# Kernel optimization log

Measured on AMD Instinct MI355X. Metric: run time of the kernel, lower is better.

Reference implementation:

```python
import jax, jax.numpy as jnp
import numpy as np

D = 1024   # embed_dim
H = 16     # n_heads
DH = D // H
B, N = 4, 1024


def setup_inputs() -> dict:
    key = jax.random.key(0)
    k0, k1, k2 = jax.random.split(key, 3)
    x = jax.random.normal(k0, (B, N, D), jnp.float32)
    # Per-head kqv Linear weights batched: each head maps D -> 2*D + D//H
    Wkqv = jax.random.normal(k1, (H, D, 2 * D + DH), jnp.float32) * 0.02
    bkqv = jnp.zeros((H, 2 * D + DH), jnp.float32)
    Wp = jax.random.normal(k2, (D, D), jnp.float32) * 0.02
    bp = jnp.zeros((D,), jnp.float32)
    return {"x": x, "Wkqv": Wkqv, "bkqv": bkqv, "Wp": Wp, "bp": bp}


def reference(x, Wkqv, bkqv, Wp, bp):
    Bm, Nm, Dm = x.shape
    # batched per-head projections: y[b,h,n,:] = x[b,n,:] @ Wkqv[h] + bkqv[h]
    y = jnp.einsum('bnd,hde->bhne', x, Wkqv) + bkqv[None, :, None, :]
    k = y[..., :Dm]          # [B,H,N,D]  (full embed_dim per head, as in source)
    q = y[..., Dm:2 * Dm]    # [B,H,N,D]
    v = y[..., 2 * Dm:]      # [B,H,N,DH]
    # attention_scores: q @ k^T / sqrt(D) -- scale uses FULL embed_dim (faithful)
    A = jnp.einsum('bhnd,bhmd->bhnm', q, k) / jnp.sqrt(jnp.float32(Dm))
    mask = jnp.tril(jnp.ones((Nm, Nm), dtype=bool))
    A = jnp.where(mask[None, None], A, -jnp.inf)
    A = jax.nn.softmax(A, axis=-1)
    sa = jnp.einsum('bhnm,bhmd->bnhd', A, v).reshape(Bm, Nm, Dm)
    return sa @ Wp + bp
```

## Files before the change

### kernel.cpp

```cpp
#include <hip/hip_runtime.h>
#include <hip/hip_bf16.h>

#define B_ 4
#define N_ 1024
#define D_ 1024
#define H_ 16
#define DH_ 64
#define E_ 2112
#define ROWS_ 4096

typedef __bf16 bf16_t;
typedef bf16_t bf16x4 __attribute__((ext_vector_type(4)));
typedef bf16_t bf16x8 __attribute__((ext_vector_type(8)));
typedef float f32x4 __attribute__((ext_vector_type(4)));

__device__ __forceinline__ void gload_lds16(const void* g, void* l) {
  __builtin_amdgcn_global_load_lds(
      (const __attribute__((address_space(1))) void*)g,
      (__attribute__((address_space(3))) void*)l, 16, 0, 0);
}

__global__ __launch_bounds__(256)
void conv_x(const float* __restrict__ x, bf16_t* __restrict__ xb) {
  const int n4 = ROWS_ * D_ / 4;
  for (int i = blockIdx.x * 256 + threadIdx.x; i < n4; i += gridDim.x * 256) {
    float4 v = ((const float4*)x)[i];
    bf16x4 o = {(bf16_t)v.x, (bf16_t)v.y, (bf16_t)v.z, (bf16_t)v.w};
    ((bf16x4*)xb)[i] = o;
  }
}

__global__ __launch_bounds__(256)
void conv_wqk(const float* __restrict__ W, const float* __restrict__ bkqv,
              bf16_t* __restrict__ Wqb, bf16_t* __restrict__ Wkb,
              float* __restrict__ wqbk, float* __restrict__ wkbq) {
  const int db = blockIdx.x;
  const int h = blockIdx.y;
  const float* Wh = W + (size_t)h * D_ * E_;
  __shared__ float bq[1024], bk[1024];
  __shared__ float red[2][16][17];
  const int t = threadIdx.x;
  for (int i = t; i < 1024; i += 256) {
    bk[i] = bkqv[h * E_ + i];
    bq[i] = bkqv[h * E_ + 1024 + i];
  }
  __syncthreads();
  const int rt = t >> 4, ct = t & 15;
  const int d = db * 16 + rt;
  const float* rowp = Wh + (size_t)d * E_;
  float pk = 0.f, pq = 0.f;
  #pragma unroll
  for (int j = 0; j < 16; ++j) {
    int e4 = (ct + j * 16) * 4;
    float4 vk = *(const float4*)(rowp + e4);
    float4 vq = *(const float4*)(rowp + 1024 + e4);
    bf16x4 ok = {(bf16_t)vk.x, (bf16_t)vk.y, (bf16_t)vk.z, (bf16_t)vk.w};
    bf16x4 oq = {(bf16_t)vq.x, (bf16_t)vq.y, (bf16_t)vq.z, (bf16_t)vq.w};
    *(bf16x4*)(Wkb + ((size_t)h * 1024 + d) * 1024 + e4) = ok;
    *(bf16x4*)(Wqb + ((size_t)h * 1024 + d) * 1024 + e4) = oq;
    pk += vk.x * bq[e4] + vk.y * bq[e4 + 1] + vk.z * bq[e4 + 2] + vk.w * bq[e4 + 3];
    pq += vq.x * bk[e4] + vq.y * bk[e4 + 1] + vq.z * bk[e4 + 2] + vq.w * bk[e4 + 3];
  }
  red[0][rt][ct] = pk;
  red[1][rt][ct] = pq;
  __syncthreads();
  if (t < 32) {
    int which = t >> 4, r = t & 15;
    float s = 0.f;
    #pragma unroll
    for (int c2 = 0; c2 < 16; ++c2) s += red[which][r][c2];
    if (which == 0) wkbq[h * 1024 + db * 16 + r] = s;
    else            wqbk[h * 1024 + db * 16 + r] = s;
  }
}

__global__ __launch_bounds__(256)
void bqk_kernel(const float* __restrict__ bkqv, float* __restrict__ bqk) {
  const int h = blockIdx.x;
  const int t = threadIdx.x;
  __shared__ float red[256];
  const float* bk = bkqv + h * E_;
  const float* bq = bk + 1024;
  float4 a = *(const float4*)(bk + t * 4);
  float4 b = *(const float4*)(bq + t * 4);
  red[t] = a.x * b.x + a.y * b.y + a.z * b.z + a.w * b.w;
  __syncthreads();
  for (int st = 128; st > 0; st >>= 1) {
    if (t < st) red[t] += red[t + st];
    __syncthreads();
  }
  if (t == 0) bqk[h] = red[0];
}

__global__ __launch_bounds__(256)
void uv_kernel(const float* __restrict__ x, const float* __restrict__ bqk,
               const float* __restrict__ wqbk, const float* __restrict__ wkbq,
               float* __restrict__ u, float* __restrict__ v) {
  const int t = threadIdx.x;
  const int w = t >> 6, l = t & 63;
  const int rg = blockIdx.x * 4 + w;
  const int b = rg >> 10, n = rg & 1023;
  const float* xr = x + (size_t)rg * 1024 + l * 16;
  float4 xv0 = *(const float4*)(xr);
  float4 xv1 = *(const float4*)(xr + 4);
  float4 xv2 = *(const float4*)(xr + 8);
  float4 xv3 = *(const float4*)(xr + 12);
  #pragma unroll
  for (int h = 0; h < 16; ++h) {
    const float* wq = wqbk + h * 1024 + l * 16;
    const float* wk = wkbq + h * 1024 + l * 16;
    float4 q0 = *(const float4*)(wq);
    float4 q1 = *(const float4*)(wq + 4);
    float4 q2 = *(const float4*)(wq + 8);
    float4 q3 = *(const float4*)(wq + 12);
    float4 k0 = *(const float4*)(wk);
    float4 k1 = *(const float4*)(wk + 4);
    float4 k2 = *(const float4*)(wk + 8);
    float4 k3 = *(const float4*)(wk + 12);
    float au = xv0.x * q0.x + xv0.y * q0.y + xv0.z * q0.z + xv0.w * q0.w
             + xv1.x * q1.x + xv1.y * q1.y + xv1.z * q1.z + xv1.w * q1.w
             + xv2.x * q2.x + xv2.y * q2.y + xv2.z * q2.z + xv2.w * q2.w
             + xv3.x * q3.x + xv3.y * q3.y + xv3.z * q3.z + xv3.w * q3.w;
    float av = xv0.x * k0.x + xv0.y * k0.y + xv0.z * k0.z + xv0.w * k0.w
             + xv1.x * k1.x + xv1.y * k1.y + xv1.z * k1.z + xv1.w * k1.w
             + xv2.x * k2.x + xv2.y * k2.y + xv2.z * k2.z + xv2.w * k2.w
             + xv3.x * k3.x + xv3.y * k3.y + xv3.z * k3.z + xv3.w * k3.w;
    #pragma unroll
    for (int s = 1; s < 64; s <<= 1) {
      au += __shfl_xor(au, s);
      av += __shfl_xor(av, s);
    }
    if (l == 0) {
      int bh = b * 16 + h;
      u[(size_t)bh * 1024 + n] = au + bqk[h];
      v[(size_t)bh * 1024 + n] = av;
    }
  }
}

__global__ __launch_bounds__(256)
void conv_wv(const float* __restrict__ W, bf16_t* __restrict__ Wvt) {
  const int et = blockIdx.x, dt = blockIdx.y, h = blockIdx.z;
  const int tx = threadIdx.x & 31, ty = threadIdx.x >> 5;
  __shared__ float tile[32][33];
  const float* Wh = W + (size_t)h * D_ * E_;
  #pragma unroll
  for (int rr = 0; rr < 4; ++rr) {
    int d = dt * 32 + rr * 8 + ty;
    int dh = et * 32 + tx;
    tile[rr * 8 + ty][tx] = Wh[(size_t)d * E_ + 2048 + dh];
  }
  __syncthreads();
  bf16_t* Wvo = Wvt + (size_t)h * DH_ * D_;
  #pragma unroll
  for (int rr = 0; rr < 4; ++rr) {
    int dh = et * 32 + rr * 8 + ty;
    int d = dt * 32 + tx;
    Wvo[(size_t)dh * D_ + d] = (bf16_t)tile[tx][rr * 8 + ty];
  }
}

__global__ __launch_bounds__(256)
void conv_wp(const float* __restrict__ Wp, bf16_t* __restrict__ Wpt) {
  const int nt = blockIdx.x, kt = blockIdx.y;
  const int tx = threadIdx.x & 31, ty = threadIdx.x >> 5;
  __shared__ float tile[32][33];
  #pragma unroll
  for (int rr = 0; rr < 4; ++rr)
    tile[rr * 8 + ty][tx] = Wp[(size_t)(kt * 32 + rr * 8 + ty) * D_ + nt * 32 + tx];
  __syncthreads();
  #pragma unroll
  for (int rr = 0; rr < 4; ++rr)
    Wpt[(size_t)(nt * 32 + rr * 8 + ty) * D_ + kt * 32 + tx] = (bf16_t)tile[tx][rr * 8 + ty];
}

__global__ __launch_bounds__(256)
void v_gemm(const bf16_t* __restrict__ xb, const bf16_t* __restrict__ Wvt,
            const float* __restrict__ bkqv, bf16_t* __restrict__ Vt) {
  const int nt = blockIdx.x;
  const int h = blockIdx.y;
  const int t = threadIdx.x;
  const int w = t >> 6, l = t & 63, l15 = l & 15, lg = l >> 4;

  __shared__ bf16_t As2[64 * 64];
  __shared__ bf16_t Bs2[128 * 64];
  const bf16_t* Wvh = Wvt + (size_t)h * DH_ * D_;
  const bf16_t* Bn = xb + (size_t)nt * 128 * D_;

  f32x4 acc[4][2] = {};
  const int rswz = (l15 & 7) << 4;

  for (int kb = 0; kb < 16; ++kb) {
    __syncthreads();
    #pragma unroll
    for (int i = 0; i < 2; ++i) {
      int idx = t + i * 256;
      int row = idx >> 3, c = idx & 7;
      gload_lds16(Wvh + (size_t)row * D_ + kb * 64 + ((c ^ (row & 7)) << 3),
                  (char*)As2 + idx * 16);
    }
    #pragma unroll
    for (int i = 0; i < 4; ++i) {
      int idx = t + i * 256;
      int row = idx >> 3, c = idx & 7;
      gload_lds16(Bn + (size_t)row * D_ + kb * 64 + ((c ^ (row & 7)) << 3),
                  (char*)Bs2 + idx * 16);
    }
    __syncthreads();
    #pragma unroll
    for (int ks = 0; ks < 2; ++ks) {
      const int cswz = (ks * 64 + lg * 16) ^ rswz;
      bf16x8 a[4], b[2];
      #pragma unroll
      for (int mi = 0; mi < 4; ++mi)
        a[mi] = *(const bf16x8*)((const char*)As2 + (mi * 16 + l15) * 128 + cswz);
      #pragma unroll
      for (int ni = 0; ni < 2; ++ni)
        b[ni] = *(const bf16x8*)((const char*)Bs2 + (w * 32 + ni * 16 + l15) * 128 + cswz);
      #pragma unroll
      for (int mi = 0; mi < 4; ++mi)
        #pragma unroll
        for (int ni = 0; ni < 2; ++ni)
          acc[mi][ni] = __builtin_amdgcn_mfma_f32_16x16x32_bf16(a[mi], b[ni], acc[mi][ni], 0, 0, 0);
    }
  }

  #pragma unroll
  for (int mi = 0; mi < 4; ++mi)
    #pragma unroll
    for (int r = 0; r < 4; ++r) {
      int dh = mi * 16 + lg * 4 + r;
      float bias = bkqv[h * E_ + 2048 + dh];
      #pragma unroll
      for (int ni = 0; ni < 2; ++ni) {
        int nn = nt * 128 + w * 32 + ni * 16 + l15;
        int b = nn >> 10, n = nn & (N_ - 1);
        int bh = b * H_ + h;
        Vt[((size_t)bh * DH_ + dh) * N_ + n] = (bf16_t)(acc[mi][ni][r] + bias);
      }
    }
}

#define WV8 asm volatile("s_waitcnt vmcnt(8)" ::: "memory")
#define WV2 asm volatile("s_waitcnt vmcnt(2)" ::: "memory")
#define WV0 asm volatile("s_waitcnt vmcnt(0)" ::: "memory")
#define WNONE

__device__ __forceinline__ void mm256_core(const bf16_t* __restrict__ Ag,
                                           const bf16_t* __restrict__ Bg,
                                           bf16_t* lds, f32x4 (&acc)[8][4]) {
  char* Asp = (char*)lds;
  char* Bsp = (char*)lds + 65536;
  const int t = threadIdx.x;
  const int w = t >> 6, l = t & 63, l15 = l & 15, lg = l >> 4;
  const int wm = w >> 2, wn = w & 3;

  const int lr = l >> 3;
  const int scol = ((l & 7) ^ lr) << 3;
  const bf16_t* bS = Bg + (size_t)(w * 8 + lr) * 1024 + scol;
  const int idxA = w * 8 + lr;
  const bf16_t* aS0 = Ag + (size_t)((idxA >> 4) * 32 + (idxA & 15)) * 1024 + scol;
  const bf16_t* aS1 = aS0 + (size_t)128 * 1024;

#define STG_B(bufi, hh, ktv)                                                   \
  do {                                                                         \
    gload_lds16(bS + (size_t)((hh) * 128) * 1024 + (ktv) * 64,                 \
                Bsp + (bufi) * 32768 + (hh) * 16384 + w * 1024);               \
    gload_lds16(bS + (size_t)((hh) * 128 + 64) * 1024 + (ktv) * 64,            \
                Bsp + (bufi) * 32768 + (hh) * 16384 + 8192 + w * 1024);        \
  } while (0)
#define STG_A(bufi, hh, ktv)                                                   \
  do {                                                                         \
    gload_lds16(aS0 + (size_t)((hh) * 16) * 1024 + (ktv) * 64,                 \
                Asp + (bufi) * 32768 + (hh) * 16384 + w * 1024);               \
    gload_lds16(aS1 + (size_t)((hh) * 16) * 1024 + (ktv) * 64,                 \
                Asp + (bufi) * 32768 + (hh) * 16384 + 8192 + w * 1024);        \
  } while (0)

  STG_B(0, 0, 0); STG_B(0, 1, 0);
  STG_A(0, 0, 0); STG_A(0, 1, 0);
  STG_B(1, 0, 1); STG_B(1, 1, 1);
  STG_A(1, 0, 1);
  WV8;
  __builtin_amdgcn_s_barrier();

  const int rswz = (l15 & 7) << 4;
  const int bro = ((wn & 1) * 64 + l15) * 128;

#define TILE_STEP(KT, SA1, SB, SA0, W1, W3)                                    \
  {                                                                            \
    const int kb_ = (KT) & 1;                                                  \
    const char* Ab = Asp + kb_ * 32768;                                        \
    const char* Bb = Bsp + kb_ * 32768 + (wn >> 1) * 16384;                    \
    bf16x8 b0[4], b1[4];                                                       \
    {                                                                          \
      const int cs = (lg * 16) ^ rswz;                                         \
      bf16x8 a[4];                                                             \
      _Pragma("unroll") for (int ni = 0; ni < 4; ++ni)                         \
        b0[ni] = *(const bf16x8*)(Bb + bro + ni * 2048 + cs);                  \
      _Pragma("unroll") for (int q = 0; q < 4; ++q)                            \
        a[q] = *(const bf16x8*)(Ab + ((wm * 4 + q) * 16 + l15) * 128 + cs);    \
      if (SA1) STG_A(((KT) + 1) & 1, 1, (KT) + 1);                             \
      asm volatile("s_waitcnt lgkmcnt(0)" ::: "memory");                       \
      __builtin_amdgcn_s_setprio(1);                                           \
      _Pragma("unroll") for (int q = 0; q < 4; ++q)                            \
        _Pragma("unroll") for (int ni = 0; ni < 4; ++ni)                       \
          acc[2 * q][ni] = __builtin_amdgcn_mfma_f32_16x16x32_bf16(            \
              a[q], b0[ni], acc[2 * q][ni], 0, 0, 0);                          \
      __builtin_amdgcn_s_setprio(0);                                           \
      __builtin_amdgcn_s_barrier();                                            \
    }                                                                          \
    {                                                                          \
      const int cs = (64 + lg * 16) ^ rswz;                                    \
      bf16x8 a[4];                                                             \
      _Pragma("unroll") for (int ni = 0; ni < 4; ++ni)                         \
        b1[ni] = *(const bf16x8*)(Bb + bro + ni * 2048 + cs);                  \
      _Pragma("unroll") for (int q = 0; q < 4; ++q)                            \
        a[q] = *(const bf16x8*)(Ab + ((wm * 4 + q) * 16 + l15) * 128 + cs);    \
      asm volatile("s_waitcnt lgkmcnt(0)" ::: "memory");                       \
      __builtin_amdgcn_s_setprio(1);                                           \
      _Pragma("unroll") for (int q = 0; q < 4; ++q)                            \
        _Pragma("unroll") for (int ni = 0; ni < 4; ++ni)                       \
          acc[2 * q][ni] = __builtin_amdgcn_mfma_f32_16x16x32_bf16(            \
              a[q], b1[ni], acc[2 * q][ni], 0, 0, 0);                          \
      __builtin_amdgcn_s_setprio(0);                                           \
      W1;                                                                      \
      __builtin_amdgcn_s_barrier();                                            \
    }                                                                          \
    {                                                                          \
      const int cs = (lg * 16) ^ rswz;                                         \
      bf16x8 a[4];                                                             \
      _Pragma("unroll") for (int q = 0; q < 4; ++q)                            \
        a[q] = *(const bf16x8*)(Ab + 16384 + ((wm * 4 + q) * 16 + l15) * 128 + cs); \
      if (SB) { STG_B((KT) & 1, 0, (KT) + 2); STG_B((KT) & 1, 1, (KT) + 2); }  \
      asm volatile("s_waitcnt lgkmcnt(0)" ::: "memory");                       \
      __builtin_amdgcn_s_setprio(1);                                           \
      _Pragma("unroll") for (int q = 0; q < 4; ++q)                            \
        _Pragma("unroll") for (int ni = 0; ni < 4; ++ni)                       \
          acc[2 * q + 1][ni] = __builtin_amdgcn_mfma_f32_16x16x32_bf16(        \
              a[q], b0[ni], acc[2 * q + 1][ni], 0, 0, 0);                      \
      __builtin_amdgcn_s_setprio(0);                                           \
      __builtin_amdgcn_s_barrier();                                            \
    }                                                                          \
    {                                                                          \
      const int cs = (64 + lg * 16) ^ rswz;                                    \
      bf16x8 a[4];                                                             \
      _Pragma("unroll") for (int q = 0; q < 4; ++q)                            \
        a[q] = *(const bf16x8*)(Ab + 16384 + ((wm * 4 + q) * 16 + l15) * 128 + cs); \
      if (SA0) STG_A((KT) & 1, 0, (KT) + 2);                                   \
      asm volatile("s_waitcnt lgkmcnt(0)" ::: "memory");                       \
      __builtin_amdgcn_s_setprio(1);                                           \
      _Pragma("unroll") for (int q = 0; q < 4; ++q)                            \
        _Pragma("unroll") for (int ni = 0; ni < 4; ++ni)                       \
          acc[2 * q + 1][ni] = __builtin_amdgcn_mfma_f32_16x16x32_bf16(        \
              a[q], b1[ni], acc[2 * q + 1][ni], 0, 0, 0);                      \
      __builtin_amdgcn_s_setprio(0);                                           \
      W3;                                                                      \
      __builtin_amdgcn_s_barrier();                                            \
    }                                                                          \
  }

  for (int kt = 0; kt < 14; ++kt) TILE_STEP(kt, 1, 1, 1, WV8, WV8);
  TILE_STEP(14, 1, 0, 0, WV8, WV2);
  TILE_STEP(15, 0, 0, 0, WV0, WNONE);

#undef TILE_STEP
#undef STG_A
#undef STG_B
}

__device__ __forceinline__ int xchunk4(int colf) {
  int c = colf >> 2;
  return ((c ^ (c >> 3)) << 2) | (colf & 3);
}

__device__ __forceinline__ void epi256_bf16(f32x4 (&acc)[8][4], bf16_t* lds,
                                            bf16_t* dst) {
  const int t = threadIdx.x;
  const int l = t & 63, l15 = l & 15, lg = l >> 4;
  const int w = t >> 6;
  const int wm = w >> 2, wn = w & 3;
  float* Ct = (float*)lds;
  const int cpair = t & 31;
  const int p0 = xchunk4(cpair * 8);
  const int p1 = xchunk4(cpair * 8 + 4);
  #pragma unroll
  for (int s = 0; s < 4; ++s) {
    __syncthreads();
    #pragma unroll
    for (int m2 = 0; m2 < 2; ++m2)
      #pragma unroll
      for (int ni = 0; ni < 4; ++ni)
        #pragma unroll
        for (int r = 0; r < 4; ++r)
          Ct[(wm * 32 + m2 * 16 + lg * 4 + r) * 258 +
             xchunk4(wn * 64 + ni * 16 + l15)] = acc[2 * s + m2][ni][r];
    __syncthreads();
    #pragma unroll
    for (int it = 0; it < 4; ++it) {
      int row64 = (t >> 5) + it * 16;
      int wmq = row64 >> 5, m2q = (row64 >> 4) & 1, r16 = row64 & 15;
      int c8 = cpair * 8;
      const float* r0 = &Ct[row64 * 258 + p0];
      const float* r1 = &Ct[row64 * 258 + p1];
      bf16x8 o = {(bf16_t)r0[0], (bf16_t)r0[1], (bf16_t)r0[2], (bf16_t)r0[3],
                  (bf16_t)r1[0], (bf16_t)r1[1], (bf16_t)r1[2], (bf16_t)r1[3]};
      int lrow = wmq * 128 + (2 * s + m2q) * 16 + r16;
      *(bf16x8*)(dst + (size_t)lrow * 1024 + c8) = o;
    }
  }
}

__global__ __launch_bounds__(512)
void m_gemm(const bf16_t* __restrict__ Wkb, const bf16_t* __restrict__ Wqb,
            bf16_t* __restrict__ MT) {
  __shared__ bf16_t lds[65536];
  const int bid = blockIdx.x;
  const int mb = bid & 3, nb = (bid >> 2) & 3, h = bid >> 4;
  f32x4 acc[8][4] = {};
  mm256_core(Wkb + ((size_t)h * 1024 + mb * 256) * 1024,
             Wqb + ((size_t)h * 1024 + nb * 256) * 1024, lds, acc);
  epi256_bf16(acc, lds,
              MT + ((size_t)h * 1024 + mb * 256) * 1024 + nb * 256);
}

__global__ __launch_bounds__(512)
void t_gemm(const bf16_t* __restrict__ xb, const bf16_t* __restrict__ MT,
            bf16_t* __restrict__ T) {
  __shared__ bf16_t lds[65536];
  const int bid = blockIdx.x;
  const int lid = (bid & 7) * 128 + (bid >> 3);
  const int mb = lid & 15, nb = (lid >> 4) & 3, h = lid >> 6;
  f32x4 acc[8][4] = {};
  mm256_core(xb + (size_t)mb * 256 * 1024,
             MT + ((size_t)h * 1024 + nb * 256) * 1024, lds, acc);
  const int b = mb >> 2;
  const int bh = b * 16 + h;
  epi256_bf16(acc, lds,
              T + (size_t)bh * 1024 * 1024 + (size_t)((mb & 3) * 256) * 1024 +
                  nb * 256);
}

__global__ __launch_bounds__(512)
void s_gemm256(const bf16_t* __restrict__ T, const bf16_t* __restrict__ xb,
               const float* __restrict__ u, const float* __restrict__ v,
               float* __restrict__ SgC, int bh0) {
  __shared__ bf16_t lds[65536];
  const int bid = blockIdx.x;
  const int lid = (bid & 7) * 40 + (bid >> 3);
  const int idx = lid % 10;
  const int bhl = lid / 10;
  const int bh = bh0 + bhl;
  const int bb = bh >> 4;
  int qt = 0;
  while ((qt + 1) * (qt + 2) / 2 <= idx) ++qt;
  const int kt = idx - qt * (qt + 1) / 2;

  f32x4 acc[8][4] = {};
  mm256_core(T + (size_t)bh * 1024 * 1024 + (size_t)qt * 256 * 1024,
             xb + (size_t)bb * 1024 * 1024 + (size_t)kt * 256 * 1024, lds, acc);

  const int t = threadIdx.x;
  const int w = t >> 6, l = t & 63, l15 = l & 15, lg = l >> 4;
  const int wm = w >> 2, wn = w & 3;
  const float SCALE = 0.045084220027780106f;
  float* So = SgC + (((size_t)bhl * 10 + idx) << 16);

  const float* ubh = u + (size_t)bh * 1024 + qt * 256;
  const float* vbh = v + (size_t)bh * 1024 + kt * 256;
  float vv[4];
  #pragma unroll
  for (int ni = 0; ni < 4; ++ni) vv[ni] = vbh[wn * 64 + ni * 16 + l15];

  #pragma unroll
  for (int mi = 0; mi < 8; ++mi)
    #pragma unroll
    for (int r = 0; r < 4; ++r) {
      int rl = wm * 128 + mi * 16 + lg * 4 + r;
      float uu = ubh[rl];
      #pragma unroll
      for (int ni = 0; ni < 4; ++ni) {
        int cl = wn * 64 + ni * 16 + l15;
        float z = (acc[mi][ni][r] + uu + vv[ni]) * SCALE;
        if (kt * 256 + cl > qt * 256 + rl) z = -1e30f;
        acc[mi][ni][r] = z;
      }
    }

  float* Ct = (float*)lds;
  const int cpair = t & 31;
  const int p0 = xchunk4(cpair * 8);
  const int p1 = xchunk4(cpair * 8 + 4);
  #pragma unroll
  for (int s = 0; s < 4; ++s) {
    __syncthreads();
    #pragma unroll
    for (int m2 = 0; m2 < 2; ++m2)
      #pragma unroll
      for (int ni = 0; ni < 4; ++ni)
        #pragma unroll
        for (int r = 0; r < 4; ++r)
          Ct[(wm * 32 + m2 * 16 + lg * 4 + r) * 258 +
             xchunk4(wn * 64 + ni * 16 + l15)] = acc[2 * s + m2][ni][r];
    __syncthreads();
    #pragma unroll
    for (int it = 0; it < 4; ++it) {
      int row64 = (t >> 5) + it * 16;
      int wmq = row64 >> 5, m2q = (row64 >> 4) & 1, r16 = row64 & 15;
      int c8 = cpair * 8;
      const float* r0 = &Ct[row64 * 258 + p0];
      const float* r1 = &Ct[row64 * 258 + p1];
      float4 v0 = {r0[0], r0[1], r0[2], r0[3]};
      float4 v1 = {r1[0], r1[1], r1[2], r1[3]};
      int rl = wmq * 128 + (2 * s + m2q) * 16 + r16;
      *(float4*)(So + (size_t)rl * 256 + c8) = v0;
      *(float4*)(So + (size_t)rl * 256 + c8 + 4) = v1;
    }
  }
}

__global__ __launch_bounds__(256)
void softmax_pv(const float* __restrict__ SgC, const bf16_t* __restrict__ Vt,
                bf16_t* __restrict__ sa, int bh0) {
  const int qt = blockIdx.x;
  const int bhl = blockIdx.y;
  const int t = threadIdx.x;
  const int w = t >> 6, l = t & 63, l15 = l & 15, lg = l >> 4;
  const int bh = bh0 + bhl;
  const int b = bh >> 4, h = bh & 15;

  const int qrow = qt * 64 + w * 16 + l15;
  const int qt8 = qt >> 2;
  const float* Sbh = SgC + (((size_t)bhl * 10) << 16);
  const bf16_t* Vh = Vt + (size_t)bh * DH_ * N_;

  f32x4 accO[4] = {};
  float m = -1e30f, lsum = 0.f;

  for (int j = 0; j <= qt; ++j) {
    const int jb = j * 64;
    const int tid = qt8 * (qt8 + 1) / 2 + (j >> 2);
    const float* Srow = Sbh + ((size_t)tid << 16) + (size_t)(qrow & 255) * 256 + (jb & 255);

    float4 sA = *(const float4*)(Srow + lg * 8);
    float4 sB = *(const float4*)(Srow + lg * 8 + 4);
    float4 sC = *(const float4*)(Srow + 32 + lg * 8);
    float4 sD = *(const float4*)(Srow + 32 + lg * 8 + 4);

    float zm = fmaxf(fmaxf(fmaxf(sA.x, sA.y), fmaxf(sA.z, sA.w)),
                     fmaxf(fmaxf(sB.x, sB.y), fmaxf(sB.z, sB.w)));
    zm = fmaxf(zm, fmaxf(fmaxf(fmaxf(sC.x, sC.y), fmaxf(sC.z, sC.w)),
                         fmaxf(fmaxf(sD.x, sD.y), fmaxf(sD.z, sD.w))));
    zm = fmaxf(zm, __shfl_xor(zm, 16));
    zm = fmaxf(zm, __shfl_xor(zm, 32));

    float mnew = fmaxf(m, zm);
    float scl = exp2f(m - mnew);
    m = mnew;

    float p[16];
    p[0] = exp2f(sA.x - mnew); p[1] = exp2f(sA.y - mnew);
    p[2] = exp2f(sA.z - mnew); p[3] = exp2f(sA.w - mnew);
    p[4] = exp2f(sB.x - mnew); p[5] = exp2f(sB.y - mnew);
    p[6] = exp2f(sB.z - mnew); p[7] = exp2f(sB.w - mnew);
    p[8] = exp2f(sC.x - mnew); p[9] = exp2f(sC.y - mnew);
    p[10] = exp2f(sC.z - mnew); p[11] = exp2f(sC.w - mnew);
    p[12] = exp2f(sD.x - mnew); p[13] = exp2f(sD.y - mnew);
    p[14] = exp2f(sD.z - mnew); p[15] = exp2f(sD.w - mnew);

    float rs = 0.f;
    #pragma unroll
    for (int i = 0; i < 16; ++i) rs += p[i];
    rs += __shfl_xor(rs, 16);
    rs += __shfl_xor(rs, 32);
    lsum = lsum * scl + rs;

    float sclO[4];
    #pragma unroll
    for (int r = 0; r < 4; ++r) sclO[r] = __shfl(scl, lg * 4 + r);
    #pragma unroll
    for (int db = 0; db < 4; ++db)
      #pragma unroll
      for (int r = 0; r < 4; ++r) accO[db][r] *= sclO[r];

    bf16x8 pa0 = {(bf16_t)p[0], (bf16_t)p[1], (bf16_t)p[2], (bf16_t)p[3],
                  (bf16_t)p[4], (bf16_t)p[5], (bf16_t)p[6], (bf16_t)p[7]};
    bf16x8 pa1 = {(bf16_t)p[8], (bf16_t)p[9], (bf16_t)p[10], (bf16_t)p[11],
                  (bf16_t)p[12], (bf16_t)p[13], (bf16_t)p[14], (bf16_t)p[15]};

    #pragma unroll
    for (int db = 0; db < 4; ++db) {
      const bf16_t* vp = Vh + (size_t)(db * 16 + l15) * N_ + jb;
      bf16x8 vb0 = *(const bf16x8*)(vp + lg * 8);
      bf16x8 vb1 = *(const bf16x8*)(vp + 32 + lg * 8);
      accO[db] = __builtin_amdgcn_mfma_f32_16x16x32_bf16(pa0, vb0, accO[db], 0, 0, 0);
      accO[db] = __builtin_amdgcn_mfma_f32_16x16x32_bf16(pa1, vb1, accO[db], 0, 0, 0);
    }
  }

  float lO[4];
  #pragma unroll
  for (int r = 0; r < 4; ++r) lO[r] = __shfl(lsum, lg * 4 + r);

  #pragma unroll
  for (int db = 0; db < 4; ++db)
    #pragma unroll
    for (int r = 0; r < 4; ++r) {
      int row = qt * 64 + w * 16 + lg * 4 + r;
      int col = h * DH_ + db * 16 + l15;
      sa[((size_t)b * N_ + row) * D_ + col] = (bf16_t)(accO[db][r] / lO[r]);
    }
}

__global__ __launch_bounds__(256)
void out_gemm(const bf16_t* __restrict__ A, const bf16_t* __restrict__ Bt,
              const float* __restrict__ bp, float* __restrict__ out) {
  const int mb = blockIdx.x, nb = blockIdx.y;
  const int t = threadIdx.x;
  const int w = t >> 6, l = t & 63, l15 = l & 15, lg = l >> 4;
  const int wr = (w >> 1) * 64, wc = (w & 1) * 64;

  __shared__ bf16_t As[128 * 64];
  __shared__ bf16_t Bs[128 * 64];

  const int srow = w * 32 + (l >> 3);
  const int scol = (l & 7) * 8;
  const bf16_t* ag = A + (size_t)(mb * 128 + srow) * D_ + scol;
  const bf16_t* bg = Bt + (size_t)(nb * 128 + srow) * D_ + scol;
  char* asl = (char*)As + w * 4096;
  char* bsl = (char*)Bs + w * 4096;

  f32x4 acc[4][4] = {};

  for (int kb = 0; kb < 16; ++kb) {
    __syncthreads();
    #pragma unroll
    for (int i = 0; i < 4; ++i) {
      gload_lds16(ag + (size_t)i * 8 * D_ + kb * 64, asl + i * 1024);
      gload_lds16(bg + (size_t)i * 8 * D_ + kb * 64, bsl + i * 1024);
    }
    __syncthreads();
    #pragma unroll
    for (int ks = 0; ks < 2; ++ks) {
      bf16x8 a[4], b[4];
      #pragma unroll
      for (int mi = 0; mi < 4; ++mi)
        a[mi] = *(const bf16x8*)((const char*)As + (wr + mi * 16 + l15) * 128 + ks * 64 + lg * 16);
      #pragma unroll
      for (int ni = 0; ni < 4; ++ni)
        b[ni] = *(const bf16x8*)((const char*)Bs + (wc + ni * 16 + l15) * 128 + ks * 64 + lg * 16);
      #pragma unroll
      for (int mi = 0; mi < 4; ++mi)
        #pragma unroll
        for (int ni = 0; ni < 4; ++ni)
          acc[mi][ni] = __builtin_amdgcn_mfma_f32_16x16x32_bf16(a[mi], b[ni], acc[mi][ni], 0, 0, 0);
    }
  }

  #pragma unroll
  for (int ni = 0; ni < 4; ++ni) {
    int e = nb * 128 + wc + ni * 16 + l15;
    float bias = bp[e];
    #pragma unroll
    for (int mi = 0; mi < 4; ++mi)
      #pragma unroll
      for (int r = 0; r < 4; ++r) {
        int grow = mb * 128 + wr + mi * 16 + lg * 4 + r;
        out[(size_t)grow * D_ + e] = acc[mi][ni][r] + bias;
      }
  }
}

extern "C" void kernel_launch(void* const* d_in, const int* in_sizes, int n_in,
                              void* d_out, int out_size, void* d_ws, size_t ws_size,
                              hipStream_t stream) {
  const float* x    = (const float*)d_in[0];
  const float* Wkqv = (const float*)d_in[1];
  const float* bkqv = (const float*)d_in[2];
  const float* Wp   = (const float*)d_in[3];
  const float* bp   = (const float*)d_in[4];
  float* out = (float*)d_out;
  char* ws = (char*)d_ws;

  const size_t MB = 1 << 20;
  bf16_t* xb   = (bf16_t*)(ws);
  bf16_t* sa   = (bf16_t*)(ws + 8 * MB);
  bf16_t* Wpt  = (bf16_t*)(ws + 16 * MB);
  bf16_t* Vt   = (bf16_t*)(ws + 18 * MB);
  bf16_t* Wvt  = (bf16_t*)(ws + 26 * MB);
  bf16_t* MT   = (bf16_t*)(ws + 28 * MB);
  bf16_t* T    = (bf16_t*)(ws + 60 * MB);
  bf16_t* Wqb  = (bf16_t*)(ws + 188 * MB);
  bf16_t* Wkb  = (bf16_t*)(ws + 220 * MB);
  float*  SgC  = (float*) (ws + 188 * MB);
  float*  u    = (float*) (ws + 268 * MB);
  float*  v    = (float*) (ws + 268 * MB + 256 * 1024);
  float*  wqbk = (float*) (ws + 268 * MB + 512 * 1024);
  float*  wkbq = (float*) (ws + 268 * MB + 576 * 1024);
  float*  bqk  = (float*) (ws + 268 * MB + 640 * 1024);

  hipLaunchKernelGGL(conv_x, dim3(1024), dim3(256), 0, stream, x, xb);
  hipLaunchKernelGGL(conv_wp, dim3(32, 32), dim3(256), 0, stream, Wp, Wpt);
  hipLaunchKernelGGL(conv_wv, dim3(2, 32, 16), dim3(256), 0, stream, Wkqv, Wvt);
  hipLaunchKernelGGL(v_gemm, dim3(32, 16), dim3(256), 0, stream, xb, Wvt, bkqv, Vt);

  hipLaunchKernelGGL(conv_wqk, dim3(64, 16), dim3(256), 0, stream,
                     Wkqv, bkqv, Wqb, Wkb, wqbk, wkbq);
  hipLaunchKernelGGL(bqk_kernel, dim3(16), dim3(256), 0, stream, bkqv, bqk);
  hipLaunchKernelGGL(uv_kernel, dim3(1024), dim3(256), 0, stream,
                     x, bqk, wqbk, wkbq, u, v);
  hipLaunchKernelGGL(m_gemm, dim3(256), dim3(512), 0, stream, Wkb, Wqb, MT);
  hipLaunchKernelGGL(t_gemm, dim3(1024), dim3(512), 0, stream, xb, MT, T);

  for (int c = 0; c < 2; ++c) {
    hipLaunchKernelGGL(s_gemm256, dim3(320), dim3(512), 0, stream,
                       T, xb, u, v, SgC, c * 32);
    hipLaunchKernelGGL(softmax_pv, dim3(16, 32), dim3(256), 0, stream,
                       SgC, Vt, sa, c * 32);
  }

  hipLaunchKernelGGL(out_gemm, dim3(32, 8), dim3(256), 0, stream, sa, Wpt, bp, out);
}
```

Baseline: 516.8 us.

## Store attention scores in bf16, drop chunking, and merge prep kernels

```diff
diff --git a/kernel.cpp b/kernel.cpp
--- a/kernel.cpp
+++ b/kernel.cpp
@@ -21,12 +21,65 @@
 }
 
 __global__ __launch_bounds__(256)
-void conv_x(const float* __restrict__ x, bf16_t* __restrict__ xb) {
-  const int n4 = ROWS_ * D_ / 4;
-  for (int i = blockIdx.x * 256 + threadIdx.x; i < n4; i += gridDim.x * 256) {
-    float4 v = ((const float4*)x)[i];
-    bf16x4 o = {(bf16_t)v.x, (bf16_t)v.y, (bf16_t)v.z, (bf16_t)v.w};
-    ((bf16x4*)xb)[i] = o;
+void prep_all(const float* __restrict__ x, const float* __restrict__ Wp,
+              const float* __restrict__ W, const float* __restrict__ bkqv,
+              bf16_t* __restrict__ xb, bf16_t* __restrict__ Wpt,
+              bf16_t* __restrict__ Wvt, float* __restrict__ bqk) {
+  __shared__ float smem[1056];
+  const int bid = blockIdx.x;
+  const int t = threadIdx.x;
+  if (bid < 1024) {
+    const int n4 = ROWS_ * D_ / 4;
+    for (int i = bid * 256 + t; i < n4; i += 1024 * 256) {
+      float4 v = ((const float4*)x)[i];
+      bf16x4 o = {(bf16_t)v.x, (bf16_t)v.y, (bf16_t)v.z, (bf16_t)v.w};
+      ((bf16x4*)xb)[i] = o;
+    }
+  } else if (bid < 2048) {
+    const int id = bid - 1024;
+    const int nt = id & 31, kt = id >> 5;
+    const int tx = t & 31, ty = t >> 5;
+    #pragma unroll
+    for (int rr = 0; rr < 4; ++rr)
+      smem[(rr * 8 + ty) * 33 + tx] =
+          Wp[(size_t)(kt * 32 + rr * 8 + ty) * D_ + nt * 32 + tx];
+    __syncthreads();
+    #pragma unroll
+    for (int rr = 0; rr < 4; ++rr)
+      Wpt[(size_t)(nt * 32 + rr * 8 + ty) * D_ + kt * 32 + tx] =
+          (bf16_t)smem[tx * 33 + rr * 8 + ty];
+  } else if (bid < 3072) {
+    const int id = bid - 2048;
+    const int et = id & 1, dt = (id >> 1) & 31, h = id >> 6;
+    const int tx = t & 31, ty = t >> 5;
+    const float* Wh = W + (size_t)h * D_ * E_;
+    #pragma unroll
+    for (int rr = 0; rr < 4; ++rr) {
+      int d = dt * 32 + rr * 8 + ty;
+      int dh = et * 32 + tx;
+      smem[(rr * 8 + ty) * 33 + tx] = Wh[(size_t)d * E_ + 2048 + dh];
+    }
+    __syncthreads();
+    bf16_t* Wvo = Wvt + (size_t)h * DH_ * D_;
+    #pragma unroll
+    for (int rr = 0; rr < 4; ++rr) {
+      int dh = et * 32 + rr * 8 + ty;
+      int d = dt * 32 + tx;
+      Wvo[(size_t)dh * D_ + d] = (bf16_t)smem[tx * 33 + rr * 8 + ty];
+    }
+  } else {
+    const int h = bid - 3072;
+    const float* bk = bkqv + h * E_;
+    const float* bq = bk + 1024;
+    float4 a = *(const float4*)(bk + t * 4);
+    float4 b = *(const float4*)(bq + t * 4);
+    smem[t] = a.x * b.x + a.y * b.y + a.z * b.z + a.w * b.w;
+    __syncthreads();
+    for (int st = 128; st > 0; st >>= 1) {
+      if (t < st) smem[t] += smem[t + st];
+      __syncthreads();
+    }
+    if (t == 0) bqk[h] = smem[0];
   }
 }
 
@@ -72,24 +125,6 @@
     if (which == 0) wkbq[h * 1024 + db * 16 + r] = s;
     else            wqbk[h * 1024 + db * 16 + r] = s;
   }
-}
-
-__global__ __launch_bounds__(256)
-void bqk_kernel(const float* __restrict__ bkqv, float* __restrict__ bqk) {
-  const int h = blockIdx.x;
-  const int t = threadIdx.x;
-  __shared__ float red[256];
-  const float* bk = bkqv + h * E_;
-  const float* bq = bk + 1024;
-  float4 a = *(const float4*)(bk + t * 4);
-  float4 b = *(const float4*)(bq + t * 4);
-  red[t] = a.x * b.x + a.y * b.y + a.z * b.z + a.w * b.w;
-  __syncthreads();
-  for (int st = 128; st > 0; st >>= 1) {
-    if (t < st) red[t] += red[t + st];
-    __syncthreads();
-  }
-  if (t == 0) bqk[h] = red[0];
 }
 
 __global__ __launch_bounds__(256)
@@ -136,42 +171,6 @@
       v[(size_t)bh * 1024 + n] = av;
     }
   }
-}
-
-__global__ __launch_bounds__(256)
-void conv_wv(const float* __restrict__ W, bf16_t* __restrict__ Wvt) {
-  const int et = blockIdx.x, dt = blockIdx.y, h = blockIdx.z;
-  const int tx = threadIdx.x & 31, ty = threadIdx.x >> 5;
-  __shared__ float tile[32][33];
-  const float* Wh = W + (size_t)h * D_ * E_;
-  #pragma unroll
-  for (int rr = 0; rr < 4; ++rr) {
-    int d = dt * 32 + rr * 8 + ty;
-    int dh = et * 32 + tx;
-    tile[rr * 8 + ty][tx] = Wh[(size_t)d * E_ + 2048 + dh];
-  }
-  __syncthreads();
-  bf16_t* Wvo = Wvt + (size_t)h * DH_ * D_;
-  #pragma unroll
-  for (int rr = 0; rr < 4; ++rr) {
-    int dh = et * 32 + rr * 8 + ty;
-    int d = dt * 32 + tx;
-    Wvo[(size_t)dh * D_ + d] = (bf16_t)tile[tx][rr * 8 + ty];
-  }
-}
-
-__global__ __launch_bounds__(256)
-void conv_wp(const float* __restrict__ Wp, bf16_t* __restrict__ Wpt) {
-  const int nt = blockIdx.x, kt = blockIdx.y;
-  const int tx = threadIdx.x & 31, ty = threadIdx.x >> 5;
-  __shared__ float tile[32][33];
-  #pragma unroll
-  for (int rr = 0; rr < 4; ++rr)
-    tile[rr * 8 + ty][tx] = Wp[(size_t)(kt * 32 + rr * 8 + ty) * D_ + nt * 32 + tx];
-  __syncthreads();
-  #pragma unroll
-  for (int rr = 0; rr < 4; ++rr)
-    Wpt[(size_t)(nt * 32 + rr * 8 + ty) * D_ + kt * 32 + tx] = (bf16_t)tile[tx][rr * 8 + ty];
 }
 
 __global__ __launch_bounds__(256)
@@ -444,13 +443,12 @@
 __global__ __launch_bounds__(512)
 void s_gemm256(const bf16_t* __restrict__ T, const bf16_t* __restrict__ xb,
                const float* __restrict__ u, const float* __restrict__ v,
-               float* __restrict__ SgC, int bh0) {
+               bf16_t* __restrict__ Sg) {
   __shared__ bf16_t lds[65536];
   const int bid = blockIdx.x;
-  const int lid = (bid & 7) * 40 + (bid >> 3);
+  const int lid = (bid & 7) * 80 + (bid >> 3);
   const int idx = lid % 10;
-  const int bhl = lid / 10;
-  const int bh = bh0 + bhl;
+  const int bh = lid / 10;
   const int bb = bh >> 4;
   int qt = 0;
   while ((qt + 1) * (qt + 2) / 2 <= idx) ++qt;
@@ -464,7 +462,7 @@
   const int w = t >> 6, l = t & 63, l15 = l & 15, lg = l >> 4;
   const int wm = w >> 2, wn = w & 3;
   const float SCALE = 0.045084220027780106f;
-  float* So = SgC + (((size_t)bhl * 10 + idx) << 16);
+  bf16_t* So = Sg + (((size_t)bh * 10 + idx) << 16);
 
   const float* ubh = u + (size_t)bh * 1024 + qt * 256;
   const float* vbh = v + (size_t)bh * 1024 + kt * 256;
@@ -510,28 +508,26 @@
       int c8 = cpair * 8;
       const float* r0 = &Ct[row64 * 258 + p0];
       const float* r1 = &Ct[row64 * 258 + p1];
-      float4 v0 = {r0[0], r0[1], r0[2], r0[3]};
-      float4 v1 = {r1[0], r1[1], r1[2], r1[3]};
+      bf16x8 o = {(bf16_t)r0[0], (bf16_t)r0[1], (bf16_t)r0[2], (bf16_t)r0[3],
+                  (bf16_t)r1[0], (bf16_t)r1[1], (bf16_t)r1[2], (bf16_t)r1[3]};
       int rl = wmq * 128 + (2 * s + m2q) * 16 + r16;
-      *(float4*)(So + (size_t)rl * 256 + c8) = v0;
-      *(float4*)(So + (size_t)rl * 256 + c8 + 4) = v1;
+      *(bf16x8*)(So + (size_t)rl * 256 + c8) = o;
     }
   }
 }
 
 __global__ __launch_bounds__(256)
-void softmax_pv(const float* __restrict__ SgC, const bf16_t* __restrict__ Vt,
-                bf16_t* __restrict__ sa, int bh0) {
+void softmax_pv(const bf16_t* __restrict__ Sg, const bf16_t* __restrict__ Vt,
+                bf16_t* __restrict__ sa) {
   const int qt = blockIdx.x;
-  const int bhl = blockIdx.y;
+  const int bh = blockIdx.y;
   const int t = threadIdx.x;
   const int w = t >> 6, l = t & 63, l15 = l & 15, lg = l >> 4;
-  const int bh = bh0 + bhl;
   const int b = bh >> 4, h = bh & 15;
 
   const int qrow = qt * 64 + w * 16 + l15;
   const int qt8 = qt >> 2;
-  const float* Sbh = SgC + (((size_t)bhl * 10) << 16);
+  const bf16_t* Sbh = Sg + (((size_t)bh * 10) << 16);
   const bf16_t* Vh = Vt + (size_t)bh * DH_ * N_;
 
   f32x4 accO[4] = {};
@@ -540,17 +536,20 @@
   for (int j = 0; j <= qt; ++j) {
     const int jb = j * 64;
     const int tid = qt8 * (qt8 + 1) / 2 + (j >> 2);
-    const float* Srow = Sbh + ((size_t)tid << 16) + (size_t)(qrow & 255) * 256 + (jb & 255);
-
-    float4 sA = *(const float4*)(Srow + lg * 8);
-    float4 sB = *(const float4*)(Srow + lg * 8 + 4);
-    float4 sC = *(const float4*)(Srow + 32 + lg * 8);
-    float4 sD = *(const float4*)(Srow + 32 + lg * 8 + 4);
-
-    float zm = fmaxf(fmaxf(fmaxf(sA.x, sA.y), fmaxf(sA.z, sA.w)),
-                     fmaxf(fmaxf(sB.x, sB.y), fmaxf(sB.z, sB.w)));
-    zm = fmaxf(zm, fmaxf(fmaxf(fmaxf(sC.x, sC.y), fmaxf(sC.z, sC.w)),
-                         fmaxf(fmaxf(sD.x, sD.y), fmaxf(sD.z, sD.w))));
+    const bf16_t* Srow = Sbh + ((size_t)tid << 16) +
+                         (size_t)(qrow & 255) * 256 + (jb & 255);
+
+    bf16x8 h0 = *(const bf16x8*)(Srow + lg * 8);
+    bf16x8 h1 = *(const bf16x8*)(Srow + 32 + lg * 8);
+    float z[16];
+    #pragma unroll
+    for (int i = 0; i < 8; ++i) z[i] = (float)h0[i];
+    #pragma unroll
+    for (int i = 0; i < 8; ++i) z[8 + i] = (float)h1[i];
+
+    float zm = z[0];
+    #pragma unroll
+    for (int i = 1; i < 16; ++i) zm = fmaxf(zm, z[i]);
     zm = fmaxf(zm, __shfl_xor(zm, 16));
     zm = fmaxf(zm, __shfl_xor(zm, 32));
 
@@ -559,14 +558,8 @@
     m = mnew;
 
     float p[16];
-    p[0] = exp2f(sA.x - mnew); p[1] = exp2f(sA.y - mnew);
-    p[2] = exp2f(sA.z - mnew); p[3] = exp2f(sA.w - mnew);
-    p[4] = exp2f(sB.x - mnew); p[5] = exp2f(sB.y - mnew);
-    p[6] = exp2f(sB.z - mnew); p[7] = exp2f(sB.w - mnew);
-    p[8] = exp2f(sC.x - mnew); p[9] = exp2f(sC.y - mnew);
-    p[10] = exp2f(sC.z - mnew); p[11] = exp2f(sC.w - mnew);
-    p[12] = exp2f(sD.x - mnew); p[13] = exp2f(sD.y - mnew);
-    p[14] = exp2f(sD.z - mnew); p[15] = exp2f(sD.w - mnew);
+    #pragma unroll
+    for (int i = 0; i < 16; ++i) p[i] = exp2f(z[i] - mnew);
 
     float rs = 0.f;
     #pragma unroll
@@ -692,32 +685,27 @@
   bf16_t* T    = (bf16_t*)(ws + 60 * MB);
   bf16_t* Wqb  = (bf16_t*)(ws + 188 * MB);
   bf16_t* Wkb  = (bf16_t*)(ws + 220 * MB);
-  float*  SgC  = (float*) (ws + 188 * MB);
+  bf16_t* Sg   = (bf16_t*)(ws + 188 * MB);
   float*  u    = (float*) (ws + 268 * MB);
   float*  v    = (float*) (ws + 268 * MB + 256 * 1024);
   float*  wqbk = (float*) (ws + 268 * MB + 512 * 1024);
   float*  wkbq = (float*) (ws + 268 * MB + 576 * 1024);
   float*  bqk  = (float*) (ws + 268 * MB + 640 * 1024);
 
-  hipLaunchKernelGGL(conv_x, dim3(1024), dim3(256), 0, stream, x, xb);
-  hipLaunchKernelGGL(conv_wp, dim3(32, 32), dim3(256), 0, stream, Wp, Wpt);
-  hipLaunchKernelGGL(conv_wv, dim3(2, 32, 16), dim3(256), 0, stream, Wkqv, Wvt);
-  hipLaunchKernelGGL(v_gemm, dim3(32, 16), dim3(256), 0, stream, xb, Wvt, bkqv, Vt);
-
+  hipLaunchKernelGGL(prep_all, dim3(3088), dim3(256), 0, stream,
+                     x, Wp, Wkqv, bkqv, xb, Wpt, Wvt, bqk);
   hipLaunchKernelGGL(conv_wqk, dim3(64, 16), dim3(256), 0, stream,
                      Wkqv, bkqv, Wqb, Wkb, wqbk, wkbq);
-  hipLaunchKernelGGL(bqk_kernel, dim3(16), dim3(256), 0, stream, bkqv, bqk);
   hipLaunchKernelGGL(uv_kernel, dim3(1024), dim3(256), 0, stream,
                      x, bqk, wqbk, wkbq, u, v);
+  hipLaunchKernelGGL(v_gemm, dim3(32, 16), dim3(256), 0, stream,
+                     xb, Wvt, bkqv, Vt);
   hipLaunchKernelGGL(m_gemm, dim3(256), dim3(512), 0, stream, Wkb, Wqb, MT);
   hipLaunchKernelGGL(t_gemm, dim3(1024), dim3(512), 0, stream, xb, MT, T);
-
-  for (int c = 0; c < 2; ++c) {
-    hipLaunchKernelGGL(s_gemm256, dim3(320), dim3(512), 0, stream,
-                       T, xb, u, v, SgC, c * 32);
-    hipLaunchKernelGGL(softmax_pv, dim3(16, 32), dim3(256), 0, stream,
-                       SgC, Vt, sa, c * 32);
-  }
-
-  hipLaunchKernelGGL(out_gemm, dim3(32, 8), dim3(256), 0, stream, sa, Wpt, bp, out);
-}
+  hipLaunchKernelGGL(s_gemm256, dim3(640), dim3(512), 0, stream,
+                     T, xb, u, v, Sg);
+  hipLaunchKernelGGL(softmax_pv, dim3(16, 64), dim3(256), 0, stream,
+                     Sg, Vt, sa);
+  hipLaunchKernelGGL(out_gemm, dim3(32, 8), dim3(256), 0, stream,
+                     sa, Wpt, bp, out);
+}
```

After: 450.0 us. 12.9% less time.
